# Kernel optimization log

Measured on AMD Instinct MI355X. Metric: run time of the kernel, lower is better.

## Reference

```python
import jax, jax.numpy as jnp
import numpy as np

KS = 3
ST = 1


def _windows(x, ks, st):
    """im2col sliding windows: (bs, c, h, w) -> (bs, c, H', W', ks, ks)
    where windows[b,c,i,j,k,f] = x[b,c, i*st+k, j*st+f] (matches torch as_strided)."""
    bs, c, h, w = x.shape
    Hp = (h - ks) // st + 1
    Wp = (w - ks) // st + 1
    return jnp.stack(
        [jnp.stack([x[:, :, k:k + Hp * st:st, f:f + Wp * st:st] for f in range(ks)], axis=-1)
         for k in range(ks)], axis=-2)


def setup_inputs() -> dict:
    key = jax.random.key(0)
    k1, k2, k3 = jax.random.split(key, 3)
    x = jax.random.normal(k1, (16, 16, 64, 512), dtype=jnp.float32)
    points = jax.random.normal(k2, (16, 3, 64, 512), dtype=jnp.float32)
    kernel = jax.random.normal(k3, (32, 16, 4), dtype=jnp.float32) * 0.05
    return {"x": x, "kernel": kernel, "points": points}


def reference(x, kernel, points):
    ks, st = KS, ST
    # (bs, in_c, H', W', ks, ks) overlapping patches of features and xyz coords
    strided_x = _windows(x, ks, st)
    strided_pts = _windows(points, ks, st)
    bd = ks // 2 if st == 1 else ks // 4
    # center point of each window: (bs, 3, H', W')
    ctr = points[:, :, bd:-bd, bd:-bd][:, :, ::st, ::st]
    # point-relative coordinates per window element: (bs, 3, H', W', ks, ks)
    rel_pts = ctr[..., None, None] - strided_pts
    # homogeneous coordinate -> d = 4
    rel_pts = jnp.concatenate([rel_pts, jnp.ones_like(rel_pts[:, :1])], axis=1)
    # kernel: (out_c, in_c, 4)
    return jnp.einsum('bdhwkf,bihwkf,oid->bohw', rel_pts, strided_x, kernel)
```

## Files before the change

kernel.cpp:

```cpp
#include <hip/hip_runtime.h>
#include <hip/hip_bf16.h>


#define HH 64
#define WW 512
#define HP 62
#define WP 510
#define IC 16
#define OC 32
#define BS 16
#define RB 4
#define TR (RB + 2)
#define TC 64
#define LC 68
#define NPL 19
#define CPR 17
#define NROWS (NPL * TR)
#define NCHUNK (NROWS * CPR)

typedef __attribute__((ext_vector_type(8))) short short8;
typedef __attribute__((ext_vector_type(4))) float f32x4;

static __device__ __forceinline__ short f2bf(float f) {
    union { __hip_bfloat16 h; short s; } u;
    u.h = __float2bfloat16(f);
    return u.s;
}

__global__ __launch_bounds__(256) void flex_conv_lds(
    const float* __restrict__ x, const float* __restrict__ kern,
    const float* __restrict__ pts, float* __restrict__ out)
{
    __shared__ float lds[NPL * TR * LC];

    const int tid = threadIdx.x;
    const int j0 = blockIdx.x * TC;
    int i0 = blockIdx.y * RB;
    if (i0 > HP - RB) i0 = HP - RB;
    const int b = blockIdx.z;

    const float* xb = x + (size_t)b * IC * HH * WW;
    const float* pb = pts + (size_t)b * 3 * HH * WW;

    #pragma unroll
    for (int rnd = 0; rnd < 8; ++rnd) {
        const int cid = tid + rnd * 256;
        if (cid < NCHUNK) {
            const int row = cid / CPR;
            const int chunk = cid - row * CPR;
            const int plane = row / TR;
            const int rr = row - plane * TR;
            const float* base = (plane < IC)
                ? (xb + (size_t)plane * HH * WW)
                : (pb + (size_t)(plane - IC) * HH * WW);
            int gcol = j0 + chunk * 4;
            if (gcol > WW - 4) gcol = WW - 4;
            const float4 v = *(const float4*)(base + (size_t)(i0 + rr) * WW + gcol);
            *(float4*)(&lds[row * LC + chunk * 4]) = v;
        }
    }
    __syncthreads();

    const int lane = tid & 63;
    const int wave = tid >> 6;
    const int p = lane & 15;
    const int c = lane >> 4;
    const int tc = wave * 16 + p;

    short8 a0lo, a0hi, a1lo, a1hi;
    {
        const float4* k0v = (const float4*)(kern + (size_t)p * 64 + c * 8);
        const float4* k1v = (const float4*)(kern + (size_t)(16 + p) * 64 + c * 8);
        float4 v0a = k0v[0], v0b = k0v[1], v0c = k0v[8], v0d = k0v[9];
        float4 v1a = k1v[0], v1b = k1v[1], v1c = k1v[8], v1d = k1v[9];
        a0lo[0]=f2bf(v0a.x); a0lo[1]=f2bf(v0a.y); a0lo[2]=f2bf(v0a.z); a0lo[3]=f2bf(v0a.w);
        a0lo[4]=f2bf(v0b.x); a0lo[5]=f2bf(v0b.y); a0lo[6]=f2bf(v0b.z); a0lo[7]=f2bf(v0b.w);
        a0hi[0]=f2bf(v0c.x); a0hi[1]=f2bf(v0c.y); a0hi[2]=f2bf(v0c.z); a0hi[3]=f2bf(v0c.w);
        a0hi[4]=f2bf(v0d.x); a0hi[5]=f2bf(v0d.y); a0hi[6]=f2bf(v0d.z); a0hi[7]=f2bf(v0d.w);
        a1lo[0]=f2bf(v1a.x); a1lo[1]=f2bf(v1a.y); a1lo[2]=f2bf(v1a.z); a1lo[3]=f2bf(v1a.w);
        a1lo[4]=f2bf(v1b.x); a1lo[5]=f2bf(v1b.y); a1lo[6]=f2bf(v1b.z); a1lo[7]=f2bf(v1b.w);
        a1hi[0]=f2bf(v1c.x); a1hi[1]=f2bf(v1c.y); a1hi[2]=f2bf(v1c.z); a1hi[3]=f2bf(v1c.w);
        a1hi[4]=f2bf(v1d.x); a1hi[5]=f2bf(v1d.y); a1hi[6]=f2bf(v1d.z); a1hi[7]=f2bf(v1d.w);
    }

    float xs[4][RB], px0[4][RB], px1[4][RB], px2[4][RB];
    #pragma unroll
    for (int t = 0; t < 4; ++t)
        #pragma unroll
        for (int q = 0; q < RB; ++q) { xs[t][q]=0.f; px0[t][q]=0.f; px1[t][q]=0.f; px2[t][q]=0.f; }
    float c0[RB], c1[RB], c2[RB];

    #pragma unroll
    for (int rr = 0; rr < TR; ++rr) {
        const float* lp0 = &lds[(IC * TR + rr) * LC + tc];
        const float* lp1 = &lds[((IC + 1) * TR + rr) * LC + tc];
        const float* lp2 = &lds[((IC + 2) * TR + rr) * LC + tc];
        const float pa0 = lp0[0], pm0 = lp0[1], pz0 = lp0[2];
        const float pa1 = lp1[0], pm1 = lp1[1], pz1 = lp1[2];
        const float pa2 = lp2[0], pm2 = lp2[1], pz2 = lp2[2];
        if (rr >= 1 && rr <= RB) { c0[rr-1] = pm0; c1[rr-1] = pm1; c2[rr-1] = pm2; }
        #pragma unroll
        for (int t = 0; t < 4; ++t) {
            const int ic = (t >> 1) * 8 + 2 * c + (t & 1);
            const float* lx = &lds[(ic * TR + rr) * LC + tc];
            const float x0 = lx[0], x1 = lx[1], x2 = lx[2];
            const float rsx = x0 + x1 + x2;
            float r0 = pa0 * x0; r0 = fmaf(pm0, x1, r0); r0 = fmaf(pz0, x2, r0);
            float r1 = pa1 * x0; r1 = fmaf(pm1, x1, r1); r1 = fmaf(pz1, x2, r1);
            float r2 = pa2 * x0; r2 = fmaf(pm2, x1, r2); r2 = fmaf(pz2, x2, r2);
            #pragma unroll
            for (int q = 0; q < RB; ++q) {
                if (rr >= q && rr <= q + 2) {
                    xs[t][q] += rsx; px0[t][q] += r0; px1[t][q] += r1; px2[t][q] += r2;
                }
            }
        }
    }

    const int j = j0 + tc;
    #pragma unroll
    for (int q = 0; q < RB; ++q) {
        short8 blo, bhi;
        #pragma unroll
        for (int t = 0; t < 4; ++t) {
            const short t0 = f2bf(fmaf(c0[q], xs[t][q], -px0[t][q]));
            const short t1 = f2bf(fmaf(c1[q], xs[t][q], -px1[t][q]));
            const short t2 = f2bf(fmaf(c2[q], xs[t][q], -px2[t][q]));
            const short t3 = f2bf(xs[t][q]);
            const int s = (t & 1) * 4;
            if (t < 2) { blo[s+0]=t0; blo[s+1]=t1; blo[s+2]=t2; blo[s+3]=t3; }
            else       { bhi[s+0]=t0; bhi[s+1]=t1; bhi[s+2]=t2; bhi[s+3]=t3; }
        }
        f32x4 acc0 = {0.f,0.f,0.f,0.f}, acc1 = {0.f,0.f,0.f,0.f};
        acc0 = __builtin_amdgcn_mfma_f32_16x16x32_bf16(a0lo, blo, acc0, 0, 0, 0);
        acc0 = __builtin_amdgcn_mfma_f32_16x16x32_bf16(a0hi, bhi, acc0, 0, 0, 0);
        acc1 = __builtin_amdgcn_mfma_f32_16x16x32_bf16(a1lo, blo, acc1, 0, 0, 0);
        acc1 = __builtin_amdgcn_mfma_f32_16x16x32_bf16(a1hi, bhi, acc1, 0, 0, 0);
        if (j < WP) {
            float* ob = out + (size_t)b * OC * HP * WP + (size_t)(i0 + q) * WP + j;
            #pragma unroll
            for (int r = 0; r < 4; ++r) {
                const int o = c * 4 + r;
                ob[(size_t)o * HP * WP]        = acc0[r];
                ob[(size_t)(o + 16) * HP * WP] = acc1[r];
            }
        }
    }
}

extern "C" void kernel_launch(void* const* d_in, const int* in_sizes, int n_in,
                              void* d_out, int out_size, void* d_ws, size_t ws_size,
                              hipStream_t stream)
{
    const float* x    = (const float*)d_in[0];
    const float* kern = (const float*)d_in[1];
    const float* pts  = (const float*)d_in[2];
    float* out = (float*)d_out;

    dim3 block(256, 1, 1);
    dim3 grid(WW / TC, (HP + RB - 1) / RB, BS);
    flex_conv_lds<<<grid, block, 0, stream>>>(x, kern, pts, out);
}
```

Before: 117.6 us.

## Pipeline row-group staging with async global-to-LDS loads over four row tiles

```diff
diff --git a/kernel.cpp b/kernel.cpp
--- a/kernel.cpp
+++ b/kernel.cpp
@@ -10,13 +10,15 @@
 #define OC 32
 #define BS 16
 #define RB 4
-#define TR (RB + 2)
 #define TC 64
-#define LC 68
+#define LCW 68
+#define CPR 17
 #define NPL 19
-#define CPR 17
-#define NROWS (NPL * TR)
-#define NCHUNK (NROWS * CPR)
+#define RPF (NPL * LCW)
+#define GRPF (4 * RPF)
+#define NGC (4 * NPL * CPR)
+#define NSLOT 3
+#define NTILE 4
 
 typedef __attribute__((ext_vector_type(8))) short short8;
 typedef __attribute__((ext_vector_type(4))) float f32x4;
@@ -27,39 +29,52 @@
     return u.s;
 }
 
-__global__ __launch_bounds__(256) void flex_conv_lds(
-    const float* __restrict__ x, const float* __restrict__ kern,
-    const float* __restrict__ pts, float* __restrict__ out)
+static __device__ __forceinline__ void stage_group(
+    const float* __restrict__ xb, const float* __restrict__ pb,
+    float* lds, int g, int j0, int tid)
 {
-    __shared__ float lds[NPL * TR * LC];
-
-    const int tid = threadIdx.x;
-    const int j0 = blockIdx.x * TC;
-    int i0 = blockIdx.y * RB;
-    if (i0 > HP - RB) i0 = HP - RB;
-    const int b = blockIdx.z;
-
-    const float* xb = x + (size_t)b * IC * HH * WW;
-    const float* pb = pts + (size_t)b * 3 * HH * WW;
-
+    float* slotbase = lds + (g % NSLOT) * GRPF;
     #pragma unroll
-    for (int rnd = 0; rnd < 8; ++rnd) {
+    for (int rnd = 0; rnd < 6; ++rnd) {
         const int cid = tid + rnd * 256;
-        if (cid < NCHUNK) {
-            const int row = cid / CPR;
-            const int chunk = cid - row * CPR;
-            const int plane = row / TR;
-            const int rr = row - plane * TR;
+        if (cid < NGC) {
+            const int r = cid / (NPL * CPR);
+            const int rem = cid - r * (NPL * CPR);
+            const int plane = rem / CPR;
+            const int chunk = rem - plane * CPR;
             const float* base = (plane < IC)
                 ? (xb + (size_t)plane * HH * WW)
                 : (pb + (size_t)(plane - IC) * HH * WW);
             int gcol = j0 + chunk * 4;
             if (gcol > WW - 4) gcol = WW - 4;
-            const float4 v = *(const float4*)(base + (size_t)(i0 + rr) * WW + gcol);
-            *(float4*)(&lds[row * LC + chunk * 4]) = v;
-        }
-    }
-    __syncthreads();
+            const float* src = base + (size_t)(g * 4 + r) * WW + gcol;
+            __builtin_amdgcn_global_load_lds(
+                (const __attribute__((address_space(1))) void*)src,
+                (__attribute__((address_space(3))) void*)(slotbase + cid * 4),
+                16, 0, 0);
+        }
+    }
+}
+
+__global__ __launch_bounds__(256) void flex_conv_pipe(
+    const float* __restrict__ x, const float* __restrict__ kern,
+    const float* __restrict__ pts, float* __restrict__ out)
+{
+    __shared__ float lds[NSLOT * GRPF];
+
+    const int tid = threadIdx.x;
+    const int j0 = blockIdx.x * TC;
+    const int ch = blockIdx.y;
+    const int b = blockIdx.z;
+
+    const float* xb = x + (size_t)b * IC * HH * WW;
+    const float* pb = pts + (size_t)b * 3 * HH * WW;
+
+    const int g0 = 4 * ch;
+    const int gend = (ch == 3) ? 15 : (g0 + 4);
+
+    stage_group(xb, pb, lds, g0, j0, tid);
+    stage_group(xb, pb, lds, g0 + 1, j0, tid);
 
     const int lane = tid & 63;
     const int wave = tid >> 6;
@@ -83,66 +98,104 @@
         a1hi[4]=f2bf(v1d.x); a1hi[5]=f2bf(v1d.y); a1hi[6]=f2bf(v1d.z); a1hi[7]=f2bf(v1d.w);
     }
 
-    float xs[4][RB], px0[4][RB], px1[4][RB], px2[4][RB];
-    #pragma unroll
-    for (int t = 0; t < 4; ++t)
-        #pragma unroll
-        for (int q = 0; q < RB; ++q) { xs[t][q]=0.f; px0[t][q]=0.f; px1[t][q]=0.f; px2[t][q]=0.f; }
-    float c0[RB], c1[RB], c2[RB];
-
-    #pragma unroll
-    for (int rr = 0; rr < TR; ++rr) {
-        const float* lp0 = &lds[(IC * TR + rr) * LC + tc];
-        const float* lp1 = &lds[((IC + 1) * TR + rr) * LC + tc];
-        const float* lp2 = &lds[((IC + 2) * TR + rr) * LC + tc];
-        const float pa0 = lp0[0], pm0 = lp0[1], pz0 = lp0[2];
-        const float pa1 = lp1[0], pm1 = lp1[1], pz1 = lp1[2];
-        const float pa2 = lp2[0], pm2 = lp2[1], pz2 = lp2[2];
-        if (rr >= 1 && rr <= RB) { c0[rr-1] = pm0; c1[rr-1] = pm1; c2[rr-1] = pm2; }
-        #pragma unroll
-        for (int t = 0; t < 4; ++t) {
-            const int ic = (t >> 1) * 8 + 2 * c + (t & 1);
-            const float* lx = &lds[(ic * TR + rr) * LC + tc];
-            const float x0 = lx[0], x1 = lx[1], x2 = lx[2];
-            const float rsx = x0 + x1 + x2;
-            float r0 = pa0 * x0; r0 = fmaf(pm0, x1, r0); r0 = fmaf(pz0, x2, r0);
-            float r1 = pa1 * x0; r1 = fmaf(pm1, x1, r1); r1 = fmaf(pz1, x2, r1);
-            float r2 = pa2 * x0; r2 = fmaf(pm2, x1, r2); r2 = fmaf(pz2, x2, r2);
+    __syncthreads();
+
+    const int j = j0 + tc;
+    float* const ob0 = out + (size_t)b * OC * HP * WP + j;
+
+    f32x4 sa0[RB], sa1[RB];
+    int pi0 = 0;
+
+    for (int u = 0; u < NTILE; ++u) {
+        const int gpre = g0 + 2 + u;
+        if (gpre <= gend) stage_group(xb, pb, lds, gpre, j0, tid);
+
+        if (u > 0 && j < WP) {
             #pragma unroll
             for (int q = 0; q < RB; ++q) {
-                if (rr >= q && rr <= q + 2) {
-                    xs[t][q] += rsx; px0[t][q] += r0; px1[t][q] += r1; px2[t][q] += r2;
+                float* ob = ob0 + (size_t)(pi0 + q) * WP;
+                #pragma unroll
+                for (int r = 0; r < 4; ++r) {
+                    const int o = c * 4 + r;
+                    ob[(size_t)o * HP * WP]        = sa0[q][r];
+                    ob[(size_t)(o + 16) * HP * WP] = sa1[q][r];
                 }
             }
         }
-    }
-
-    const int j = j0 + tc;
-    #pragma unroll
-    for (int q = 0; q < RB; ++q) {
-        short8 blo, bhi;
-        #pragma unroll
-        for (int t = 0; t < 4; ++t) {
-            const short t0 = f2bf(fmaf(c0[q], xs[t][q], -px0[t][q]));
-            const short t1 = f2bf(fmaf(c1[q], xs[t][q], -px1[t][q]));
-            const short t2 = f2bf(fmaf(c2[q], xs[t][q], -px2[t][q]));
-            const short t3 = f2bf(xs[t][q]);
-            const int s = (t & 1) * 4;
-            if (t < 2) { blo[s+0]=t0; blo[s+1]=t1; blo[s+2]=t2; blo[s+3]=t3; }
-            else       { bhi[s+0]=t0; bhi[s+1]=t1; bhi[s+2]=t2; bhi[s+3]=t3; }
-        }
-        f32x4 acc0 = {0.f,0.f,0.f,0.f}, acc1 = {0.f,0.f,0.f,0.f};
-        acc0 = __builtin_amdgcn_mfma_f32_16x16x32_bf16(a0lo, blo, acc0, 0, 0, 0);
-        acc0 = __builtin_amdgcn_mfma_f32_16x16x32_bf16(a0hi, bhi, acc0, 0, 0, 0);
-        acc1 = __builtin_amdgcn_mfma_f32_16x16x32_bf16(a1lo, blo, acc1, 0, 0, 0);
-        acc1 = __builtin_amdgcn_mfma_f32_16x16x32_bf16(a1hi, bhi, acc1, 0, 0, 0);
-        if (j < WP) {
-            float* ob = out + (size_t)b * OC * HP * WP + (size_t)(i0 + q) * WP + j;
+
+        int i0 = 16 * ch + RB * u;
+        if (i0 > HP - RB) i0 = HP - RB;
+
+        float xs[4][RB], px0[4][RB], px1[4][RB], px2[4][RB];
+        #pragma unroll
+        for (int t = 0; t < 4; ++t)
+            #pragma unroll
+            for (int q = 0; q < RB; ++q) { xs[t][q]=0.f; px0[t][q]=0.f; px1[t][q]=0.f; px2[t][q]=0.f; }
+        float c0[RB], c1[RB], c2[RB];
+
+        #pragma unroll
+        for (int rr = 0; rr < RB + 2; ++rr) {
+            const int ir = i0 + rr;
+            const int sb = ((ir >> 2) % NSLOT) * GRPF + (ir & 3) * RPF + tc;
+            const float* lp0 = &lds[sb + (IC + 0) * LCW];
+            const float* lp1 = &lds[sb + (IC + 1) * LCW];
+            const float* lp2 = &lds[sb + (IC + 2) * LCW];
+            const float pa0 = lp0[0], pm0 = lp0[1], pz0 = lp0[2];
+            const float pa1 = lp1[0], pm1 = lp1[1], pz1 = lp1[2];
+            const float pa2 = lp2[0], pm2 = lp2[1], pz2 = lp2[2];
+            if (rr >= 1 && rr <= RB) { c0[rr-1] = pm0; c1[rr-1] = pm1; c2[rr-1] = pm2; }
+            #pragma unroll
+            for (int t = 0; t < 4; ++t) {
+                const int icp = (t >> 1) * 8 + 2 * c + (t & 1);
+                const float* lx = &lds[sb + icp * LCW];
+                const float x0 = lx[0], x1 = lx[1], x2 = lx[2];
+                const float rsx = x0 + x1 + x2;
+                float r0 = pa0 * x0; r0 = fmaf(pm0, x1, r0); r0 = fmaf(pz0, x2, r0);
+                float r1 = pa1 * x0; r1 = fmaf(pm1, x1, r1); r1 = fmaf(pz1, x2, r1);
+                float r2 = pa2 * x0; r2 = fmaf(pm2, x1, r2); r2 = fmaf(pz2, x2, r2);
+                #pragma unroll
+                for (int q = 0; q < RB; ++q) {
+                    if (rr >= q && rr <= q + 2) {
+                        xs[t][q] += rsx; px0[t][q] += r0; px1[t][q] += r1; px2[t][q] += r2;
+                    }
+                }
+            }
+        }
+
+        #pragma unroll
+        for (int q = 0; q < RB; ++q) {
+            short8 blo, bhi;
+            #pragma unroll
+            for (int t = 0; t < 4; ++t) {
+                const short t0 = f2bf(fmaf(c0[q], xs[t][q], -px0[t][q]));
+                const short t1 = f2bf(fmaf(c1[q], xs[t][q], -px1[t][q]));
+                const short t2 = f2bf(fmaf(c2[q], xs[t][q], -px2[t][q]));
+                const short t3 = f2bf(xs[t][q]);
+                const int s = (t & 1) * 4;
+                if (t < 2) { blo[s+0]=t0; blo[s+1]=t1; blo[s+2]=t2; blo[s+3]=t3; }
+                else       { bhi[s+0]=t0; bhi[s+1]=t1; bhi[s+2]=t2; bhi[s+3]=t3; }
+            }
+            f32x4 acc0 = {0.f,0.f,0.f,0.f}, acc1 = {0.f,0.f,0.f,0.f};
+            acc0 = __builtin_amdgcn_mfma_f32_16x16x32_bf16(a0lo, blo, acc0, 0, 0, 0);
+            acc0 = __builtin_amdgcn_mfma_f32_16x16x32_bf16(a0hi, bhi, acc0, 0, 0, 0);
+            acc1 = __builtin_amdgcn_mfma_f32_16x16x32_bf16(a1lo, blo, acc1, 0, 0, 0);
+            acc1 = __builtin_amdgcn_mfma_f32_16x16x32_bf16(a1hi, bhi, acc1, 0, 0, 0);
+            sa0[q] = acc0; sa1[q] = acc1;
+        }
+        pi0 = i0;
+
+        if (u + 1 < NTILE) __syncthreads();
+    }
+
+    if (j < WP) {
+        #pragma unroll
+        for (int q = 0; q < RB; ++q) {
+            float* ob = ob0 + (size_t)(pi0 + q) * WP;
             #pragma unroll
             for (int r = 0; r < 4; ++r) {
                 const int o = c * 4 + r;
-                ob[(size_t)o * HP * WP]        = acc0[r];
-                ob[(size_t)(o + 16) * HP * WP] = acc1[r];
+                ob[(size_t)o * HP * WP]        = sa0[q][r];
+                ob[(size_t)(o + 16) * HP * WP] = sa1[q][r];
             }
         }
     }
@@ -158,6 +211,6 @@
     float* out = (float*)d_out;
 
     dim3 block(256, 1, 1);
-    dim3 grid(WW / TC, (HP + RB - 1) / RB, BS);
-    flex_conv_lds<<<grid, block, 0, stream>>>(x, kern, pts, out);
-}
+    dim3 grid(WW / TC, 4, BS);
+    flex_conv_pipe<<<grid, block, 0, stream>>>(x, kern, pts, out);
+}
```

After: 116.9 us. No clear change (-0.6%).
